# Kernel optimization log

Measured on AMD Instinct MI355X. Metric: run time of the kernel, lower is better.

## Reference

```python
import jax, jax.numpy as jnp
import numpy as np

T, INPUT_DIM, HIDDEN_DIM = 4096, 512, 2048
LEAK = 0.3
SPECTRAL_RADIUS = 0.9
BIAS_SCALE = 0.0
POWER_ITERS = 20


def setup_inputs() -> dict:
    key = jax.random.key(0)
    kU, kWin, kW, kv = jax.random.split(key, 4)
    U = jax.random.normal(kU, (T, INPUT_DIM), dtype=jnp.float32)
    Win = jax.random.normal(kWin, (HIDDEN_DIM, INPUT_DIM), dtype=jnp.float32)
    W = jax.random.normal(kW, (HIDDEN_DIM, HIDDEN_DIM), dtype=jnp.float32)
    # spectral scaling via power iteration (mirrors _spectral_scale_)
    v = jax.random.normal(kv, (HIDDEN_DIM, 1), dtype=jnp.float32)
    def body(v, _):
        v = W @ v
        v = v / (jnp.linalg.norm(v) + 1e-8)
        return v, None
    v, _ = jax.lax.scan(body, v, None, length=POWER_ITERS)
    s = jnp.linalg.norm(W @ v)
    W = W * (SPECTRAL_RADIUS / s)
    bias = jnp.zeros((HIDDEN_DIM,), dtype=jnp.float32) * BIAS_SCALE
    return {"U": U, "Win": Win, "W": W, "bias": bias}


def reference(U, Win, W, bias):
    def step(h, u):
        pre = Win @ u + W @ h + bias
        h = (1.0 - LEAK) * h + LEAK * jnp.tanh(pre)
        return h, h
    h0 = jnp.zeros((W.shape[0],), dtype=U.dtype)
    _, H = jax.lax.scan(step, h0, U)  # H: (T, hidden_dim)
    return H
```

## Files before the change

### kernel.cpp

```cpp
#include <hip/hip_runtime.h>
#include <hip/hip_bf16.h>
#include <math.h>

#define T_STEPS 4096
#define IN_DIM  512
#define HID     2048
#define LEAK    0.3f

#define GBM 64
#define GBN 64
#define GBK 32

__global__ __launch_bounds__(256) void gemm_p(const float* __restrict__ U,
                                              const float* __restrict__ Win,
                                              const float* __restrict__ bias,
                                              float* __restrict__ P) {
  __shared__ float As[GBM][GBK + 1];
  __shared__ float Bs[GBN][GBK + 1];
  const int bm = blockIdx.x, bn = blockIdx.y;
  const int tid = threadIdx.x;
  const int tx = tid & 15, ty = tid >> 4;

  float acc[4][4];
#pragma unroll
  for (int m = 0; m < 4; ++m)
#pragma unroll
    for (int n = 0; n < 4; ++n) acc[m][n] = 0.f;

  const float* Ub = U + (size_t)bm * GBM * IN_DIM;
  const float* Wb = Win + (size_t)bn * GBN * IN_DIM;

  for (int k0 = 0; k0 < IN_DIM; k0 += GBK) {
#pragma unroll
    for (int v = 0; v < 2; ++v) {
      const int f4 = v * 256 + tid;
      const int row = f4 >> 3;
      const int c4 = (f4 & 7) << 2;
      const float4 a = *(const float4*)(Ub + (size_t)row * IN_DIM + k0 + c4);
      As[row][c4 + 0] = a.x; As[row][c4 + 1] = a.y;
      As[row][c4 + 2] = a.z; As[row][c4 + 3] = a.w;
      const float4 b = *(const float4*)(Wb + (size_t)row * IN_DIM + k0 + c4);
      Bs[row][c4 + 0] = b.x; Bs[row][c4 + 1] = b.y;
      Bs[row][c4 + 2] = b.z; Bs[row][c4 + 3] = b.w;
    }
    __syncthreads();
#pragma unroll 8
    for (int k = 0; k < GBK; ++k) {
      float a[4], b[4];
#pragma unroll
      for (int m = 0; m < 4; ++m) a[m] = As[ty * 4 + m][k];
#pragma unroll
      for (int n = 0; n < 4; ++n) b[n] = Bs[tx * 4 + n][k];
#pragma unroll
      for (int m = 0; m < 4; ++m)
#pragma unroll
        for (int n = 0; n < 4; ++n)
          acc[m][n] = fmaf(a[m], b[n], acc[m][n]);
    }
    __syncthreads();
  }

#pragma unroll
  for (int m = 0; m < 4; ++m) {
    const int gr = bm * GBM + ty * 4 + m;
#pragma unroll
    for (int n = 0; n < 4; ++n) {
      const int gc = bn * GBN + tx * 4 + n;
      P[(size_t)gr * HID + gc] = acc[m][n] + bias[gc];
    }
  }
}

#define NB   64
#define NT   512
#define RPB  (HID / NB)
#define TPR  (NT / RPB)
#define NF4  (HID / (TPR * 4))

__device__ __forceinline__ float fast_tanh(float x) {
  const float e = __expf(2.f * x);
  return 1.f - 2.f / (e + 1.f);
}

__device__ __forceinline__ void pub(unsigned long long* p, unsigned tag, float v) {
  const unsigned long long w =
      ((unsigned long long)tag << 32) | (unsigned long long)__float_as_uint(v);
  __hip_atomic_store(p, w, __ATOMIC_RELAXED, __HIP_MEMORY_SCOPE_AGENT);
}

__global__ __launch_bounds__(NT, 1) void esn_recur(const float* __restrict__ W,
                                                   float* __restrict__ out,
                                                   unsigned long long* __restrict__ slots) {
  const int tid = threadIdx.x;
  const int j   = tid & (TPR - 1);
  const int rl  = tid >> 4;
  const int row = blockIdx.x * RPB + rl;

  __shared__ float hs[HID];

  float4 wreg[NF4];
  const float4* wrow = (const float4*)(W + (size_t)row * HID);
#pragma unroll
  for (int i = 0; i < NF4; ++i) wreg[i] = wrow[i * TPR + j];

  float hp = LEAK * fast_tanh(out[row]);
  if (j == 0) {
    out[row] = hp;
    pub(&slots[row], 1u, hp);
  }

  for (int t = 1; t < T_STEPS; ++t) {
    float* __restrict__ ocur = out + (size_t)t * HID;
    const float p = ocur[row];

    unsigned long long* __restrict__ src = slots + (size_t)((t - 1) & 1) * HID;
    const unsigned expect = (unsigned)t;
    float4 hv4;
#pragma unroll
    for (int q = 0; q < 4; ++q) {
      unsigned long long w;
      do {
        w = __hip_atomic_load(&src[tid * 4 + q], __ATOMIC_RELAXED,
                              __HIP_MEMORY_SCOPE_AGENT);
      } while ((unsigned)(w >> 32) != expect);
      ((float*)&hv4)[q] = __uint_as_float((unsigned)(w & 0xffffffffu));
    }
    __syncthreads();
    *(float4*)&hs[tid * 4] = hv4;
    __syncthreads();

    float4 acc = make_float4(0.f, 0.f, 0.f, 0.f);
#pragma unroll
    for (int i = 0; i < NF4; ++i) {
      const float4 hv = *(const float4*)&hs[(i * TPR + j) * 4];
      acc.x = fmaf(wreg[i].x, hv.x, acc.x);
      acc.y = fmaf(wreg[i].y, hv.y, acc.y);
      acc.z = fmaf(wreg[i].z, hv.z, acc.z);
      acc.w = fmaf(wreg[i].w, hv.w, acc.w);
    }
    float a = (acc.x + acc.y) + (acc.z + acc.w);
    a += __shfl_xor(a, 1, TPR);
    a += __shfl_xor(a, 2, TPR);
    a += __shfl_xor(a, 4, TPR);
    a += __shfl_xor(a, 8, TPR);

    const float h = (1.f - LEAK) * hp + LEAK * fast_tanh(p + a);
    hp = h;
    if (j == 0) {
      ocur[row] = h;
      pub(&slots[(size_t)(t & 1) * HID + row], (unsigned)(t + 1), h);
    }
  }
}

extern "C" void kernel_launch(void* const* d_in, const int* in_sizes, int n_in,
                              void* d_out, int out_size, void* d_ws, size_t ws_size,
                              hipStream_t stream) {
  const float* U    = (const float*)d_in[0];
  const float* Win  = (const float*)d_in[1];
  const float* W    = (const float*)d_in[2];
  const float* bias = (const float*)d_in[3];
  float* out = (float*)d_out;
  unsigned long long* slots = (unsigned long long*)d_ws;

  hipMemsetAsync(d_ws, 0, 2 * HID * sizeof(unsigned long long), stream);

  dim3 ggrid(T_STEPS / GBM, HID / GBN);
  gemm_p<<<ggrid, 256, 0, stream>>>(U, Win, bias, out);

  esn_recur<<<NB, NT, 0, stream>>>(W, out, slots);
}
```

Measured before the change: 13.44 ms.

## Replace per-element tagged slots with per-wave sentinel flags and stream W from memory

Replaces the 64-bit tagged value slots, which each thread spun on per element, with plain float hidden-state buffers plus one monotonic sentinel counter per wavefront. Consumers poll a single sentinel and then read four floats. Producers fence with s_waitcnt before bumping their flag. The shared h buffer is double-buffered, which removes one __syncthreads per step. W rows are no longer kept in registers and are reloaded from global memory or cache every step. This cuts register pressure but adds memory traffic on the serial critical path, and the correctness of the relaxed-ordering flag protocol rests on the waitcnt fence.

```diff
diff --git a/kernel.cpp b/kernel.cpp
--- a/kernel.cpp
+++ b/kernel.cpp
@@ -73,8 +73,9 @@
 
 #define NB   64
 #define NT   512
+#define NW   (NT / 64)
 #define RPB  (HID / NB)
-#define TPR  (NT / RPB)
+#define TPR  16
 #define NF4  (HID / (TPR * 4))
 
 __device__ __forceinline__ float fast_tanh(float x) {
@@ -82,61 +83,61 @@
   return 1.f - 2.f / (e + 1.f);
 }
 
-__device__ __forceinline__ void pub(unsigned long long* p, unsigned tag, float v) {
-  const unsigned long long w =
-      ((unsigned long long)tag << 32) | (unsigned long long)__float_as_uint(v);
-  __hip_atomic_store(p, w, __ATOMIC_RELAXED, __HIP_MEMORY_SCOPE_AGENT);
-}
-
 __global__ __launch_bounds__(NT, 1) void esn_recur(const float* __restrict__ W,
                                                    float* __restrict__ out,
-                                                   unsigned long long* __restrict__ slots) {
-  const int tid = threadIdx.x;
-  const int j   = tid & (TPR - 1);
-  const int rl  = tid >> 4;
-  const int row = blockIdx.x * RPB + rl;
+                                                   unsigned* __restrict__ sent,
+                                                   float* __restrict__ hsl) {
+  const int tid  = threadIdx.x;
+  const int j    = tid & (TPR - 1);
+  const int rl   = tid >> 4;
+  const int row  = blockIdx.x * RPB + rl;
+  const int lane = tid & 63;
+  const int wid  = tid >> 6;
+  const int sidx = blockIdx.x * NW + wid;
 
-  __shared__ float hs[HID];
+  __shared__ float hs[2][HID];
 
-  float4 wreg[NF4];
   const float4* wrow = (const float4*)(W + (size_t)row * HID);
-#pragma unroll
-  for (int i = 0; i < NF4; ++i) wreg[i] = wrow[i * TPR + j];
 
   float hp = LEAK * fast_tanh(out[row]);
   if (j == 0) {
     out[row] = hp;
-    pub(&slots[row], 1u, hp);
+    __hip_atomic_store(&hsl[row], hp, __ATOMIC_RELAXED, __HIP_MEMORY_SCOPE_AGENT);
   }
+  asm volatile("s_waitcnt vmcnt(0)" ::: "memory");
+  if (lane == 0)
+    __hip_atomic_store(&sent[sidx], 1u, __ATOMIC_RELAXED, __HIP_MEMORY_SCOPE_AGENT);
 
   for (int t = 1; t < T_STEPS; ++t) {
     float* __restrict__ ocur = out + (size_t)t * HID;
     const float p = ocur[row];
+    asm volatile("" :: "v"(p));
 
-    unsigned long long* __restrict__ src = slots + (size_t)((t - 1) & 1) * HID;
-    const unsigned expect = (unsigned)t;
+    unsigned v;
+    do {
+      v = __hip_atomic_load(&sent[tid], __ATOMIC_RELAXED, __HIP_MEMORY_SCOPE_AGENT);
+    } while (v < (unsigned)t);
+
+    const float* __restrict__ src = hsl + (size_t)((t - 1) & 1) * HID + tid * 4;
     float4 hv4;
-#pragma unroll
-    for (int q = 0; q < 4; ++q) {
-      unsigned long long w;
-      do {
-        w = __hip_atomic_load(&src[tid * 4 + q], __ATOMIC_RELAXED,
-                              __HIP_MEMORY_SCOPE_AGENT);
-      } while ((unsigned)(w >> 32) != expect);
-      ((float*)&hv4)[q] = __uint_as_float((unsigned)(w & 0xffffffffu));
-    }
-    __syncthreads();
-    *(float4*)&hs[tid * 4] = hv4;
+    hv4.x = __hip_atomic_load(&src[0], __ATOMIC_RELAXED, __HIP_MEMORY_SCOPE_AGENT);
+    hv4.y = __hip_atomic_load(&src[1], __ATOMIC_RELAXED, __HIP_MEMORY_SCOPE_AGENT);
+    hv4.z = __hip_atomic_load(&src[2], __ATOMIC_RELAXED, __HIP_MEMORY_SCOPE_AGENT);
+    hv4.w = __hip_atomic_load(&src[3], __ATOMIC_RELAXED, __HIP_MEMORY_SCOPE_AGENT);
+
+    float* __restrict__ hb = hs[(t - 1) & 1];
+    *(float4*)&hb[tid * 4] = hv4;
     __syncthreads();
 
     float4 acc = make_float4(0.f, 0.f, 0.f, 0.f);
 #pragma unroll
     for (int i = 0; i < NF4; ++i) {
-      const float4 hv = *(const float4*)&hs[(i * TPR + j) * 4];
-      acc.x = fmaf(wreg[i].x, hv.x, acc.x);
-      acc.y = fmaf(wreg[i].y, hv.y, acc.y);
-      acc.z = fmaf(wreg[i].z, hv.z, acc.z);
-      acc.w = fmaf(wreg[i].w, hv.w, acc.w);
+      const float4 wv = wrow[i * TPR + j];
+      const float4 hv = *(const float4*)&hb[(i * TPR + j) * 4];
+      acc.x = fmaf(wv.x, hv.x, acc.x);
+      acc.y = fmaf(wv.y, hv.y, acc.y);
+      acc.z = fmaf(wv.z, hv.z, acc.z);
+      acc.w = fmaf(wv.w, hv.w, acc.w);
     }
     float a = (acc.x + acc.y) + (acc.z + acc.w);
     a += __shfl_xor(a, 1, TPR);
@@ -146,10 +147,16 @@
 
     const float h = (1.f - LEAK) * hp + LEAK * fast_tanh(p + a);
     hp = h;
+
     if (j == 0) {
       ocur[row] = h;
-      pub(&slots[(size_t)(t & 1) * HID + row], (unsigned)(t + 1), h);
+      __hip_atomic_store(&hsl[(size_t)(t & 1) * HID + row], h,
+                         __ATOMIC_RELAXED, __HIP_MEMORY_SCOPE_AGENT);
     }
+    asm volatile("s_waitcnt vmcnt(0)" ::: "memory");
+    if (lane == 0)
+      __hip_atomic_store(&sent[sidx], (unsigned)(t + 1),
+                         __ATOMIC_RELAXED, __HIP_MEMORY_SCOPE_AGENT);
   }
 }
 
@@ -161,12 +168,13 @@
   const float* W    = (const float*)d_in[2];
   const float* bias = (const float*)d_in[3];
   float* out = (float*)d_out;
-  unsigned long long* slots = (unsigned long long*)d_ws;
+  unsigned* sent = (unsigned*)d_ws;
+  float* hsl = (float*)((char*)d_ws + 4096);
 
-  hipMemsetAsync(d_ws, 0, 2 * HID * sizeof(unsigned long long), stream);
+  hipMemsetAsync(d_ws, 0, 4096 + 2 * HID * sizeof(float), stream);
 
   dim3 ggrid(T_STEPS / GBM, HID / GBN);
   gemm_p<<<ggrid, 256, 0, stream>>>(U, Win, bias, out);
 
-  esn_recur<<<NB, NT, 0, stream>>>(W, out, slots);
+  esn_recur<<<NB, NT, 0, stream>>>(W, out, sent, hsl);
 }
```

Measured after the change: 20.70 ms. 54.0% more time.
